# Kernel tuning notes

Hardware: AMD Instinct MI355X
Metric: run time of the kernel (lower is better)

The kernel has to match this reference:

```python
import jax, jax.numpy as jnp
import numpy as np

D = 1024  # input_dim


def setup_inputs() -> dict:
    key = jax.random.key(0)
    ks = jax.random.split(key, 7)
    s = 1.0 / np.sqrt(D)
    return {
        "x": jax.random.normal(ks[0], (4, 2048, D), dtype=jnp.float32),
        "wq": jax.random.normal(ks[1], (D, D), dtype=jnp.float32) * s,
        "bq": jax.random.normal(ks[2], (D,), dtype=jnp.float32) * s,
        "wk": jax.random.normal(ks[3], (D, D), dtype=jnp.float32) * s,
        "bk": jax.random.normal(ks[4], (D,), dtype=jnp.float32) * s,
        "wv": jax.random.normal(ks[5], (D, D), dtype=jnp.float32) * s,
        "bv": jax.random.normal(ks[6], (D,), dtype=jnp.float32) * s,
    }


def reference(x, wq, bq, wk, bk, wv, bv):
    # torch Linear: y = x @ W^T + b
    q = jnp.einsum('btd,ed->bte', x, wq) + bq  # (B,T,D)
    k = jnp.einsum('btd,ed->bte', x, wk) + bk
    v = jnp.einsum('btd,ed->bte', x, wv) + bv
    scale = 1.0 / jnp.sqrt(jnp.asarray(D, dtype=x.dtype))
    scores = jnp.einsum('btd,bsd->bts', q, k) * scale  # (B,T,T)
    attn = jax.nn.softmax(scores, axis=-1)
    return jnp.einsum('bts,bsd->btd', attn, v)
```

## Files before the change

### kernel.cpp

```cpp
#include <hip/hip_runtime.h>
#include <stdint.h>

#define BB 4
#define TT 2048
#define DD 1024

typedef unsigned short u16;
typedef unsigned int u32;
typedef u16 u16x4 __attribute__((ext_vector_type(4)));
typedef u16 u16x8 __attribute__((ext_vector_type(8)));
typedef float f32x4 __attribute__((ext_vector_type(4)));
typedef short s16x8 __attribute__((ext_vector_type(8)));

__device__ __forceinline__ u16 f2bf(float f) {
  u32 u = __float_as_uint(f);
  return (u16)((u + 0x7fffu + ((u >> 16) & 1u)) >> 16);
}
__device__ __forceinline__ float bf2f(u16 h) {
  return __uint_as_float((u32)h << 16);
}

__device__ __forceinline__ void gload_lds16(const void* g, void* l) {
  __builtin_amdgcn_global_load_lds(
      (const __attribute__((address_space(1))) u32*)g,
      (__attribute__((address_space(3))) u32*)l, 16, 0, 0);
}

__device__ __forceinline__ void swizzle_tiles(int& tileM, int& tileN) {
  const int gN = gridDim.x, gM = gridDim.y;
  const int L = blockIdx.y * gN + blockIdx.x;
  const int xcd = L & 7, j = L >> 3;
  const int Mq = gM >> 2, Nq = gN >> 1;
  tileM = (((xcd >> 1) * Mq) + j / Nq) << 7;
  tileN = (((xcd & 1) * Nq) + j % Nq) << 7;
}

__global__ __launch_bounds__(256) void cast_bf16_kernel(
    const float* __restrict__ in, u16* __restrict__ out, int n8) {
  int i = blockIdx.x * 256 + threadIdx.x;
  if (i >= n8) return;
  const f32x4* p = (const f32x4*)in;
  f32x4 a = p[2 * (size_t)i];
  f32x4 b = p[2 * (size_t)i + 1];
  u16x8 o;
  o[0] = f2bf(a[0]); o[1] = f2bf(a[1]); o[2] = f2bf(a[2]); o[3] = f2bf(a[3]);
  o[4] = f2bf(b[0]); o[5] = f2bf(b[1]); o[6] = f2bf(b[2]); o[7] = f2bf(b[3]);
  *(u16x8*)(out + 8 * (size_t)i) = o;
}

__global__ __launch_bounds__(256) void wcast_kernel(
    const float* __restrict__ wq, const float* __restrict__ wk,
    const float* __restrict__ wv, u16* __restrict__ out) {
  int i = blockIdx.x * 256 + threadIdx.x;
  const int n1 = DD * DD / 8;
  const float* src = i < n1 ? wq : (i < 2 * n1 ? wk : wv);
  int ii = i < n1 ? i : (i < 2 * n1 ? i - n1 : i - 2 * n1);
  const f32x4* p = (const f32x4*)src;
  f32x4 a = p[2 * (size_t)ii];
  f32x4 b = p[2 * (size_t)ii + 1];
  u16x8 o;
  o[0] = f2bf(a[0]); o[1] = f2bf(a[1]); o[2] = f2bf(a[2]); o[3] = f2bf(a[3]);
  o[4] = f2bf(b[0]); o[5] = f2bf(b[1]); o[6] = f2bf(b[2]); o[7] = f2bf(b[3]);
  *(u16x8*)(out + 8 * (size_t)i) = o;
}

__global__ __launch_bounds__(256) void bias_concat_kernel(
    const float* __restrict__ bq, const float* __restrict__ bk,
    const float* __restrict__ bv, float* __restrict__ out) {
  int i = blockIdx.x * 256 + threadIdx.x;
  float v = i < DD ? bq[i] : (i < 2 * DD ? bk[i - DD] : bv[i - 2 * DD]);
  out[i] = v;
}

__device__ __forceinline__ void kloop_bt(
    const u16* __restrict__ A, const u16* __restrict__ B, int lda, int ldb,
    int K, int tileM, int tileN, u16* sA, u16* sB, f32x4 acc[4][4]) {
  const int tid = threadIdx.x;
  const int lane = tid & 63;
  const int wave = tid >> 6;
  const int quad = lane >> 4;
  const int l15 = lane & 15;
  const int wm = (wave >> 1) << 6;
  const int wn = (wave & 1) << 6;

  const u16 *gA[4], *gB[4];
  u16 *lA[4], *lB[4];
#pragma unroll
  for (int j = 0; j < 4; ++j) {
    const int ch = wave * 256 + j * 64 + lane;
    const int r = ch >> 3;
    const int cg = ((ch & 7) ^ (r & 7)) * 8;
    gA[j] = A + (size_t)(tileM + r) * lda + cg;
    gB[j] = B + (size_t)(tileN + r) * ldb + cg;
    lA[j] = sA + wave * 2048 + j * 512;
    lB[j] = sB + wave * 2048 + j * 512;
  }

  const int x0 = (quad ^ (l15 & 7)) * 8;
  int aOff[4], bOff[4];
#pragma unroll
  for (int i = 0; i < 4; ++i) {
    aOff[i] = (wm + i * 16 + l15) * 64 + x0;
    bOff[i] = (wn + i * 16 + l15) * 64 + x0;
  }

  for (int it = 0; it < K; it += 64) {
#pragma unroll
    for (int j = 0; j < 4; ++j) gload_lds16(gA[j], lA[j]);
#pragma unroll
    for (int j = 0; j < 4; ++j) gload_lds16(gB[j], lB[j]);
#pragma unroll
    for (int j = 0; j < 4; ++j) { gA[j] += 64; gB[j] += 64; }
    __syncthreads();

    s16x8 af[4], bf[4];
#pragma unroll
    for (int i = 0; i < 4; ++i) af[i] = *(const s16x8*)(sA + aOff[i]);
#pragma unroll
    for (int i = 0; i < 4; ++i) bf[i] = *(const s16x8*)(sB + bOff[i]);
#pragma unroll
    for (int mi = 0; mi < 4; ++mi)
#pragma unroll
      for (int ni = 0; ni < 4; ++ni)
        acc[mi][ni] = __builtin_amdgcn_mfma_f32_16x16x32_bf16(
            af[mi], bf[ni], acc[mi][ni], 0, 0, 0);

#pragma unroll
    for (int i = 0; i < 4; ++i) af[i] = *(const s16x8*)(sA + (aOff[i] ^ 32));
#pragma unroll
    for (int i = 0; i < 4; ++i) bf[i] = *(const s16x8*)(sB + (bOff[i] ^ 32));
#pragma unroll
    for (int mi = 0; mi < 4; ++mi)
#pragma unroll
      for (int ni = 0; ni < 4; ++ni)
        acc[mi][ni] = __builtin_amdgcn_mfma_f32_16x16x32_bf16(
            af[mi], bf[ni], acc[mi][ni], 0, 0, 0);
    __syncthreads();
  }
}

__global__ __launch_bounds__(256, 2) void gemm_qkv(
    const u16* __restrict__ A, const u16* __restrict__ B,
    u16* __restrict__ qk, u16* __restrict__ vt, const float* __restrict__ bias) {
  __shared__ u16 sA[128 * 64];
  __shared__ u16 sB[128 * 64];
  const int lane = threadIdx.x & 63;
  const int wave = threadIdx.x >> 6;
  const int quad = lane >> 4;
  const int l15 = lane & 15;
  const int wm = (wave >> 1) << 6;
  const int wn = (wave & 1) << 6;
  int tileM, tileN;
  swizzle_tiles(tileM, tileN);

  f32x4 acc[4][4] = {};
  kloop_bt(A, B, DD, DD, DD, tileM, tileN, sA, sB, acc);

  const int rowB = tileM + wm + quad * 4;
  const int colB = tileN + wn + l15;
  if (tileN < 2048) {
    const float scale = (tileN < 1024) ? 0.03125f : 1.0f;
#pragma unroll
    for (int mi = 0; mi < 4; ++mi)
#pragma unroll
      for (int r = 0; r < 4; ++r) {
        u16* crow = qk + (size_t)(rowB + mi * 16 + r) * 2048 + colB;
#pragma unroll
        for (int ni = 0; ni < 4; ++ni)
          crow[ni * 16] = f2bf((acc[mi][ni][r] + bias[colB + ni * 16]) * scale);
      }
  } else {
    const int b = tileM >> 11;
    const int tBase = (rowB & 2047);
    u16* vb = vt + (size_t)b * DD * TT;
#pragma unroll
    for (int mi = 0; mi < 4; ++mi)
#pragma unroll
      for (int ni = 0; ni < 4; ++ni) {
        const int e = colB + ni * 16 - 2048;
        const float bs = bias[colB + ni * 16];
        u16x4 o;
#pragma unroll
        for (int r = 0; r < 4; ++r) o[r] = f2bf(acc[mi][ni][r] + bs);
        *(u16x4*)(vb + (size_t)e * TT + tBase + mi * 16) = o;
      }
  }
}

__global__ __launch_bounds__(256, 2) void gemm_s(
    const u16* __restrict__ qk, u16* __restrict__ sbuf,
    float* __restrict__ part) {
  __shared__ u16 sA[128 * 64];
  __shared__ u16 sB[128 * 64];
  const int lane = threadIdx.x & 63;
  const int wave = threadIdx.x >> 6;
  const int quad = lane >> 4;
  const int l15 = lane & 15;
  const int wm = (wave >> 1) << 6;
  const int wn = (wave & 1) << 6;
  int tileM, tileN;
  swizzle_tiles(tileM, tileN);
  const int z = blockIdx.z;

  const u16* A = qk + (size_t)z * TT * 2048;
  const u16* B = qk + (size_t)z * TT * 2048 + 1024;

  f32x4 acc[4][4] = {};
  kloop_bt(A, B, 2048, 2048, 1024, tileM, tileN, sA, sB, acc);

  const int rowB = tileM + wm + quad * 4;
  const int colB = tileN + wn + l15;
  u16* C = sbuf + (size_t)z * TT * 2048;
  const int nIdx2 = (tileN + wn) >> 6;
  float* prow = part + ((size_t)z * 32 + nIdx2) * TT;
#pragma unroll
  for (int mi = 0; mi < 4; ++mi)
#pragma unroll
    for (int r = 0; r < 4; ++r) {
      const int row = rowB + mi * 16 + r;
      u16* crow = C + (size_t)row * 2048 + colB;
      float s = 0.f;
#pragma unroll
      for (int ni = 0; ni < 4; ++ni) {
        const u16 h = f2bf(__expf(acc[mi][ni][r]));
        crow[ni * 16] = h;
        s += bf2f(h);
      }
#pragma unroll
      for (int m = 1; m <= 8; m <<= 1) s += __shfl_xor(s, m, 64);
      if (l15 == 0) prow[row] = s;
    }
}

__global__ __launch_bounds__(256, 2) void gemm_pv(
    const u16* __restrict__ sbuf, const u16* __restrict__ vt,
    float* __restrict__ out, const float* __restrict__ part) {
  __shared__ u16 sA[128 * 64];
  __shared__ u16 sB[128 * 64];
  __shared__ float rowInv[128];
  const int tid = threadIdx.x;
  const int lane = tid & 63;
  const int wave = tid >> 6;
  const int quad = lane >> 4;
  const int l15 = lane & 15;
  const int wm = (wave >> 1) << 6;
  const int wn = (wave & 1) << 6;
  int tileM, tileN;
  swizzle_tiles(tileM, tileN);
  const int z = blockIdx.z;

  if (tid < 128) {
    const float* pp = part + (size_t)z * 32 * TT + tileM + tid;
    float s = 0.f;
#pragma unroll
    for (int j = 0; j < 32; ++j) s += pp[j * TT];
    rowInv[tid] = 1.0f / s;
  }

  const u16* A = sbuf + (size_t)z * TT * 2048;
  const u16* B = vt + (size_t)z * DD * TT;

  f32x4 acc[4][4] = {};
  kloop_bt(A, B, 2048, TT, TT, tileM, tileN, sA, sB, acc);

  const int rowB = tileM + wm + quad * 4;
  const int colB = tileN + wn + l15;
  float* C = out + (size_t)z * TT * DD;
#pragma unroll
  for (int mi = 0; mi < 4; ++mi)
#pragma unroll
    for (int r = 0; r < 4; ++r) {
      const int lrow = wm + quad * 4 + mi * 16 + r;
      const float inv = rowInv[lrow];
      float* crow = C + (size_t)(rowB + mi * 16 + r) * DD + colB;
#pragma unroll
      for (int ni = 0; ni < 4; ++ni) crow[ni * 16] = acc[mi][ni][r] * inv;
    }
}

extern "C" void kernel_launch(void* const* d_in, const int* in_sizes, int n_in,
                              void* d_out, int out_size, void* d_ws,
                              size_t ws_size, hipStream_t stream) {
  const float* x = (const float*)d_in[0];
  const float* wq = (const float*)d_in[1];
  const float* bq = (const float*)d_in[2];
  const float* wk = (const float*)d_in[3];
  const float* bk = (const float*)d_in[4];
  const float* wv = (const float*)d_in[5];
  const float* bv = (const float*)d_in[6];
  float* out = (float*)d_out;

  const size_t MB = 1024 * 1024;
  if (ws_size < 103 * MB) return;
  char* ws = (char*)d_ws;
  u16* xbf = (u16*)(ws);
  float* part = (float*)(ws);
  u16* wcat = (u16*)(ws + 16 * MB);
  float* bcat = (float*)(ws + 22 * MB);
  u16* qk = (u16*)(ws + 23 * MB);
  u16* vt = (u16*)(ws + 55 * MB);
  u16* sbuf = (u16*)(ws + 71 * MB);

  const dim3 blk(256);

  cast_bf16_kernel<<<BB * TT * DD / 8 / 256, blk, 0, stream>>>(
      x, xbf, BB * TT * DD / 8);
  wcast_kernel<<<3 * DD * DD / 8 / 256, blk, 0, stream>>>(wq, wk, wv, wcat);
  bias_concat_kernel<<<12, blk, 0, stream>>>(bq, bk, bv, bcat);

  gemm_qkv<<<dim3(3 * DD / 128, BB * TT / 128, 1), blk, 0, stream>>>(
      xbf, wcat, qk, vt, bcat);

  gemm_s<<<dim3(TT / 128, TT / 128, BB), blk, 0, stream>>>(qk, sbuf, part);

  gemm_pv<<<dim3(DD / 128, TT / 128, BB), blk, 0, stream>>>(
      sbuf, vt, out, part);
}
```

Measured before the change: 236.1 us.

## Use 256x128 tiles with 8 waves and triple-buffered LDS pipeline in GEMMs

All three GEMMs move from 128x128 tiles with 4 waves to 256x128 tiles with 8 waves (512 threads). The k-loop becomes a 3-stage LDS ring buffer that prefetches two tiles ahead. Global-to-LDS loads are interleaved between MFMA quarter-blocks, with explicit waitcnt, barriers and setprio. The goal is to hide global-load latency and raise reuse of the B operand. The cost is 144 KB of LDS per block (likely one block per CU) and many more barriers, which may limit occupancy.

```diff
diff --git a/kernel.cpp b/kernel.cpp
--- a/kernel.cpp
+++ b/kernel.cpp
@@ -31,7 +31,7 @@
   const int L = blockIdx.y * gN + blockIdx.x;
   const int xcd = L & 7, j = L >> 3;
   const int Mq = gM >> 2, Nq = gN >> 1;
-  tileM = (((xcd >> 1) * Mq) + j / Nq) << 7;
+  tileM = (((xcd >> 1) * Mq) + j / Nq) << 8;
   tileN = (((xcd & 1) * Nq) + j % Nq) << 7;
 }
 
@@ -72,9 +72,33 @@
   out[i] = v;
 }
 
-__device__ __forceinline__ void kloop_bt(
+#define BUFE 24576
+
+__device__ __forceinline__ void ld2(const u16* sb, const int* off,
+                                    s16x8 out[2][2]) {
+#pragma unroll
+  for (int i = 0; i < 2; ++i) {
+    out[i][0] = *(const s16x8*)(sb + off[i]);
+    out[i][1] = *(const s16x8*)(sb + (off[i] ^ 32));
+  }
+}
+
+__device__ __forceinline__ void mfma8(const s16x8 af[2][2],
+                                      const s16x8 bf[2][2], f32x4 acc[4][4],
+                                      int mo, int no) {
+#pragma unroll
+  for (int mi = 0; mi < 2; ++mi)
+#pragma unroll
+    for (int ni = 0; ni < 2; ++ni)
+#pragma unroll
+      for (int ks = 0; ks < 2; ++ks)
+        acc[mo + mi][no + ni] = __builtin_amdgcn_mfma_f32_16x16x32_bf16(
+            af[mi][ks], bf[ni][ks], acc[mo + mi][no + ni], 0, 0, 0);
+}
+
+__device__ __forceinline__ void kloop8(
     const u16* __restrict__ A, const u16* __restrict__ B, int lda, int ldb,
-    int K, int tileM, int tileN, u16* sA, u16* sB, f32x4 acc[4][4]) {
+    int K, int tileM, int tileN, u16* sm, f32x4 acc[4][4]) {
   const int tid = threadIdx.x;
   const int lane = tid & 63;
   const int wave = tid >> 6;
@@ -83,17 +107,24 @@
   const int wm = (wave >> 1) << 6;
   const int wn = (wave & 1) << 6;
 
-  const u16 *gA[4], *gB[4];
-  u16 *lA[4], *lB[4];
+  const u16* gA[4];
+  const u16* gB[2];
+  int lA[4], lB[2];
 #pragma unroll
   for (int j = 0; j < 4; ++j) {
     const int ch = wave * 256 + j * 64 + lane;
     const int r = ch >> 3;
     const int cg = ((ch & 7) ^ (r & 7)) * 8;
     gA[j] = A + (size_t)(tileM + r) * lda + cg;
+    lA[j] = wave * 2048 + j * 512;
+  }
+#pragma unroll
+  for (int j = 0; j < 2; ++j) {
+    const int ch = wave * 128 + j * 64 + lane;
+    const int r = ch >> 3;
+    const int cg = ((ch & 7) ^ (r & 7)) * 8;
     gB[j] = B + (size_t)(tileN + r) * ldb + cg;
-    lA[j] = sA + wave * 2048 + j * 512;
-    lB[j] = sB + wave * 2048 + j * 512;
+    lB[j] = 16384 + wave * 1024 + j * 512;
   }
 
   const int x0 = (quad ^ (l15 & 7)) * 8;
@@ -101,49 +132,86 @@
 #pragma unroll
   for (int i = 0; i < 4; ++i) {
     aOff[i] = (wm + i * 16 + l15) * 64 + x0;
-    bOff[i] = (wn + i * 16 + l15) * 64 + x0;
-  }
-
-  for (int it = 0; it < K; it += 64) {
-#pragma unroll
-    for (int j = 0; j < 4; ++j) gload_lds16(gA[j], lA[j]);
-#pragma unroll
-    for (int j = 0; j < 4; ++j) gload_lds16(gB[j], lB[j]);
-#pragma unroll
-    for (int j = 0; j < 4; ++j) { gA[j] += 64; gB[j] += 64; }
-    __syncthreads();
-
-    s16x8 af[4], bf[4];
-#pragma unroll
-    for (int i = 0; i < 4; ++i) af[i] = *(const s16x8*)(sA + aOff[i]);
-#pragma unroll
-    for (int i = 0; i < 4; ++i) bf[i] = *(const s16x8*)(sB + bOff[i]);
-#pragma unroll
-    for (int mi = 0; mi < 4; ++mi)
-#pragma unroll
-      for (int ni = 0; ni < 4; ++ni)
-        acc[mi][ni] = __builtin_amdgcn_mfma_f32_16x16x32_bf16(
-            af[mi], bf[ni], acc[mi][ni], 0, 0, 0);
-
-#pragma unroll
-    for (int i = 0; i < 4; ++i) af[i] = *(const s16x8*)(sA + (aOff[i] ^ 32));
-#pragma unroll
-    for (int i = 0; i < 4; ++i) bf[i] = *(const s16x8*)(sB + (bOff[i] ^ 32));
-#pragma unroll
-    for (int mi = 0; mi < 4; ++mi)
-#pragma unroll
-      for (int ni = 0; ni < 4; ++ni)
-        acc[mi][ni] = __builtin_amdgcn_mfma_f32_16x16x32_bf16(
-            af[mi], bf[ni], acc[mi][ni], 0, 0, 0);
-    __syncthreads();
-  }
-}
-
-__global__ __launch_bounds__(256, 2) void gemm_qkv(
+    bOff[i] = 16384 + (wn + i * 16 + l15) * 64 + x0;
+  }
+
+#pragma unroll
+  for (int tb = 0; tb < 2; ++tb) {
+    u16* dst = sm + tb * BUFE;
+#pragma unroll
+    for (int j = 0; j < 4; ++j) gload_lds16(gA[j], dst + lA[j]);
+#pragma unroll
+    for (int j = 0; j < 2; ++j) gload_lds16(gB[j], dst + lB[j]);
+#pragma unroll
+    for (int j = 0; j < 4; ++j) gA[j] += 64;
+#pragma unroll
+    for (int j = 0; j < 2; ++j) gB[j] += 64;
+  }
+  asm volatile("s_waitcnt vmcnt(6)");
+  __builtin_amdgcn_s_barrier();
+
+  const int NT = K >> 6;
+  int buf = 0;
+  for (int t = 0; t < NT; ++t) {
+    const u16* sb = sm + buf * BUFE;
+    const int b2i = (buf + 2 >= 3) ? buf - 1 : buf + 2;
+    u16* st = sm + b2i * BUFE;
+    const bool stage = (t + 2 < NT);
+
+    s16x8 fa0[2][2], fb0[2][2], fa2[2][2], fb2[2][2];
+
+    ld2(sb, aOff, fa0);
+    ld2(sb, bOff, fb0);
+    if (stage) { gload_lds16(gA[0], st + lA[0]); gload_lds16(gA[1], st + lA[1]); }
+    __builtin_amdgcn_s_barrier();
+    asm volatile("s_waitcnt lgkmcnt(0)");
+    __builtin_amdgcn_s_setprio(1);
+    mfma8(fa0, fb0, acc, 0, 0);
+    __builtin_amdgcn_s_setprio(0);
+    __builtin_amdgcn_s_barrier();
+
+    ld2(sb, bOff + 2, fb2);
+    if (stage) { gload_lds16(gA[2], st + lA[2]); gload_lds16(gA[3], st + lA[3]); }
+    __builtin_amdgcn_s_barrier();
+    asm volatile("s_waitcnt lgkmcnt(0)");
+    __builtin_amdgcn_s_setprio(1);
+    mfma8(fa0, fb2, acc, 0, 2);
+    __builtin_amdgcn_s_setprio(0);
+    __builtin_amdgcn_s_barrier();
+
+    ld2(sb, aOff + 2, fa2);
+    if (stage) {
+      gload_lds16(gB[0], st + lB[0]);
+      gload_lds16(gB[1], st + lB[1]);
+#pragma unroll
+      for (int j = 0; j < 4; ++j) gA[j] += 64;
+#pragma unroll
+      for (int j = 0; j < 2; ++j) gB[j] += 64;
+    }
+    __builtin_amdgcn_s_barrier();
+    asm volatile("s_waitcnt lgkmcnt(0)");
+    __builtin_amdgcn_s_setprio(1);
+    mfma8(fa2, fb2, acc, 2, 2);
+    __builtin_amdgcn_s_setprio(0);
+    __builtin_amdgcn_s_barrier();
+
+    __builtin_amdgcn_s_setprio(1);
+    mfma8(fa2, fb0, acc, 2, 0);
+    __builtin_amdgcn_s_setprio(0);
+    if (t < NT - 2) {
+      asm volatile("s_waitcnt vmcnt(6)");
+    } else if (t == NT - 2) {
+      asm volatile("s_waitcnt vmcnt(0)");
+    }
+    __builtin_amdgcn_s_barrier();
+    buf = (buf + 1 >= 3) ? 0 : buf + 1;
+  }
+}
+
+__global__ __launch_bounds__(512, 2) void gemm_qkv(
     const u16* __restrict__ A, const u16* __restrict__ B,
     u16* __restrict__ qk, u16* __restrict__ vt, const float* __restrict__ bias) {
-  __shared__ u16 sA[128 * 64];
-  __shared__ u16 sB[128 * 64];
+  __shared__ u16 sm[3 * BUFE];
   const int lane = threadIdx.x & 63;
   const int wave = threadIdx.x >> 6;
   const int quad = lane >> 4;
@@ -154,7 +222,7 @@
   swizzle_tiles(tileM, tileN);
 
   f32x4 acc[4][4] = {};
-  kloop_bt(A, B, DD, DD, DD, tileM, tileN, sA, sB, acc);
+  kloop8(A, B, DD, DD, DD, tileM, tileN, sm, acc);
 
   const int rowB = tileM + wm + quad * 4;
   const int colB = tileN + wn + l15;
@@ -187,11 +255,10 @@
   }
 }
 
-__global__ __launch_bounds__(256, 2) void gemm_s(
+__global__ __launch_bounds__(512, 2) void gemm_s(
     const u16* __restrict__ qk, u16* __restrict__ sbuf,
     float* __restrict__ part) {
-  __shared__ u16 sA[128 * 64];
-  __shared__ u16 sB[128 * 64];
+  __shared__ u16 sm[3 * BUFE];
   const int lane = threadIdx.x & 63;
   const int wave = threadIdx.x >> 6;
   const int quad = lane >> 4;
@@ -206,7 +273,7 @@
   const u16* B = qk + (size_t)z * TT * 2048 + 1024;
 
   f32x4 acc[4][4] = {};
-  kloop_bt(A, B, 2048, 2048, 1024, tileM, tileN, sA, sB, acc);
+  kloop8(A, B, 2048, 2048, 1024, tileM, tileN, sm, acc);
 
   const int rowB = tileM + wm + quad * 4;
   const int colB = tileN + wn + l15;
@@ -232,12 +299,11 @@
     }
 }
 
-__global__ __launch_bounds__(256, 2) void gemm_pv(
+__global__ __launch_bounds__(512, 2) void gemm_pv(
     const u16* __restrict__ sbuf, const u16* __restrict__ vt,
     float* __restrict__ out, const float* __restrict__ part) {
-  __shared__ u16 sA[128 * 64];
-  __shared__ u16 sB[128 * 64];
-  __shared__ float rowInv[128];
+  __shared__ u16 sm[3 * BUFE];
+  __shared__ float rowInv[256];
   const int tid = threadIdx.x;
   const int lane = tid & 63;
   const int wave = tid >> 6;
@@ -249,19 +315,20 @@
   swizzle_tiles(tileM, tileN);
   const int z = blockIdx.z;
 
-  if (tid < 128) {
+  if (tid < 256) {
     const float* pp = part + (size_t)z * 32 * TT + tileM + tid;
     float s = 0.f;
 #pragma unroll
     for (int j = 0; j < 32; ++j) s += pp[j * TT];
     rowInv[tid] = 1.0f / s;
   }
+  __syncthreads();
 
   const u16* A = sbuf + (size_t)z * TT * 2048;
   const u16* B = vt + (size_t)z * DD * TT;
 
   f32x4 acc[4][4] = {};
-  kloop_bt(A, B, 2048, TT, TT, tileM, tileN, sA, sB, acc);
+  kloop8(A, B, 2048, TT, TT, tileM, tileN, sm, acc);
 
   const int rowB = tileM + wm + quad * 4;
   const int colB = tileN + wn + l15;
@@ -301,18 +368,19 @@
   u16* vt = (u16*)(ws + 55 * MB);
   u16* sbuf = (u16*)(ws + 71 * MB);
 
-  const dim3 blk(256);
-
-  cast_bf16_kernel<<<BB * TT * DD / 8 / 256, blk, 0, stream>>>(
+  const dim3 blk256(256);
+  const dim3 blk512(512);
+
+  cast_bf16_kernel<<<BB * TT * DD / 8 / 256, blk256, 0, stream>>>(
       x, xbf, BB * TT * DD / 8);
-  wcast_kernel<<<3 * DD * DD / 8 / 256, blk, 0, stream>>>(wq, wk, wv, wcat);
-  bias_concat_kernel<<<12, blk, 0, stream>>>(bq, bk, bv, bcat);
-
-  gemm_qkv<<<dim3(3 * DD / 128, BB * TT / 128, 1), blk, 0, stream>>>(
+  wcast_kernel<<<3 * DD * DD / 8 / 256, blk256, 0, stream>>>(wq, wk, wv, wcat);
+  bias_concat_kernel<<<12, blk256, 0, stream>>>(bq, bk, bv, bcat);
+
+  gemm_qkv<<<dim3(3 * DD / 128, BB * TT / 256, 1), blk512, 0, stream>>>(
       xbf, wcat, qk, vt, bcat);
 
-  gemm_s<<<dim3(TT / 128, TT / 128, BB), blk, 0, stream>>>(qk, sbuf, part);
-
-  gemm_pv<<<dim3(DD / 128, TT / 128, BB), blk, 0, stream>>>(
+  gemm_s<<<dim3(TT / 128, TT / 256, BB), blk512, 0, stream>>>(qk, sbuf, part);
+
+  gemm_pv<<<dim3(DD / 128, TT / 256, BB), blk512, 0, stream>>>(
       sbuf, vt, out, part);
 }
```

Measured after the change: 259.4 us. +9.9%, slower.

## Use 256-row, 8-wave GEMM tiles with interleaved load/MFMA pipeline for QKV and scores

Applied to the files above, without the earlier changes.

Adds a new 512-thread k-loop that computes 256x192 (QKV) or 256x256 (scores) tiles with double-buffered LDS. Global-to-LDS loads are split into four phases interleaved with MFMA bursts, using explicit barriers, waitcnts and setprio. The goal is more operand reuse per byte loaded and better overlap of memory with compute. It costs more LDS and registers per block, fewer blocks in the grid, and a fragile hand-written sync schedule. The PV GEMM keeps the old 128x128 path.

```diff
diff --git a/kernel.cpp b/kernel.cpp
--- a/kernel.cpp
+++ b/kernel.cpp
@@ -26,13 +26,13 @@
       (__attribute__((address_space(3))) u32*)l, 16, 0, 0);
 }
 
-__device__ __forceinline__ void swizzle_tiles(int& tileM, int& tileN) {
+__device__ __forceinline__ void swz(int BMv, int BNv, int& tileM, int& tileN) {
   const int gN = gridDim.x, gM = gridDim.y;
   const int L = blockIdx.y * gN + blockIdx.x;
   const int xcd = L & 7, j = L >> 3;
   const int Mq = gM >> 2, Nq = gN >> 1;
-  tileM = (((xcd >> 1) * Mq) + j / Nq) << 7;
-  tileN = (((xcd & 1) * Nq) + j % Nq) << 7;
+  tileM = (((xcd >> 1) * Mq) + j / Nq) * BMv;
+  tileN = (((xcd & 1) * Nq) + j % Nq) * BNv;
 }
 
 __global__ __launch_bounds__(256) void cast_bf16_kernel(
@@ -72,6 +72,163 @@
   out[i] = v;
 }
 
+template <int NR>
+__device__ __forceinline__ void kloop256(
+    const u16* __restrict__ A, const u16* __restrict__ B, int lda, int ldb,
+    int K, int tileM, int tileN, u16* sm, f32x4 (&acc)[8][NR]) {
+  constexpr int AE = 16384;
+  constexpr int BUF = AE + NR * 4096;
+  const int tid = threadIdx.x;
+  const int lane = tid & 63;
+  const int wave = tid >> 6;
+  const int quad = lane >> 4;
+  const int l15 = lane & 15;
+  const int wm = (wave >> 2) << 7;
+  const int wn = (wave & 3) * (NR * 16);
+
+  const int chl = wave * 64 + lane;
+  const int rloc = chl >> 3;
+  const int cg = ((chl & 7) ^ (rloc & 7)) * 8;
+  const int ldst = chl * 8;
+
+  const u16* gA[4];
+  const u16* gB[NR];
+#pragma unroll
+  for (int j = 0; j < 4; ++j)
+    gA[j] = A + (size_t)(tileM + j * 64 + rloc) * lda + cg;
+#pragma unroll
+  for (int j = 0; j < NR; ++j)
+    gB[j] = B + (size_t)(tileN + j * 64 + rloc) * ldb + cg;
+
+  const int x0 = (quad ^ (l15 & 7)) * 8;
+  int aOff[8];
+  int bOff[NR];
+#pragma unroll
+  for (int i = 0; i < 8; ++i) aOff[i] = (wm + i * 16 + l15) * 64 + x0;
+#pragma unroll
+  for (int i = 0; i < NR; ++i) bOff[i] = AE + (wn + i * 16 + l15) * 64 + x0;
+
+  {
+    u16* d = sm;
+    gload_lds16(gA[0], d + 0 * 4096 + ldst);
+    gload_lds16(gA[2], d + 2 * 4096 + ldst);
+#pragma unroll
+    for (int j = 0; j < NR; ++j) gload_lds16(gB[j], d + AE + j * 4096 + ldst);
+    gload_lds16(gA[1], d + 1 * 4096 + ldst);
+    gload_lds16(gA[3], d + 3 * 4096 + ldst);
+#pragma unroll
+    for (int j = 0; j < 4; ++j) gA[j] += 64;
+#pragma unroll
+    for (int j = 0; j < NR; ++j) gB[j] += 64;
+  }
+  asm volatile("s_waitcnt vmcnt(2)" ::: "memory");
+  __builtin_amdgcn_s_barrier();
+  __builtin_amdgcn_sched_barrier(0);
+
+  const int NT = K >> 6;
+  for (int t = 0; t < NT; ++t) {
+    const u16* sb = sm + (t & 1) * BUF;
+    u16* st = sm + ((t + 1) & 1) * BUF;
+    const bool stg = (t + 1 < NT);
+    s16x8 af[4], bf[NR];
+
+#pragma unroll
+    for (int i = 0; i < 4; ++i) af[i] = *(const s16x8*)(sb + aOff[i]);
+#pragma unroll
+    for (int i = 0; i < NR; ++i) bf[i] = *(const s16x8*)(sb + bOff[i]);
+    if (stg) {
+      gload_lds16(gA[0], st + 0 * 4096 + ldst);
+      gload_lds16(gA[2], st + 2 * 4096 + ldst);
+    }
+    __builtin_amdgcn_s_barrier();
+    __builtin_amdgcn_sched_barrier(0);
+    asm volatile("s_waitcnt lgkmcnt(0)" ::: "memory");
+    __builtin_amdgcn_s_setprio(1);
+#pragma unroll
+    for (int mi = 0; mi < 4; ++mi)
+#pragma unroll
+      for (int ni = 0; ni < NR; ++ni)
+        acc[mi][ni] = __builtin_amdgcn_mfma_f32_16x16x32_bf16(
+            af[mi], bf[ni], acc[mi][ni], 0, 0, 0);
+    __builtin_amdgcn_s_setprio(0);
+    if (stg) {
+      asm volatile("s_waitcnt vmcnt(2)" ::: "memory");
+    } else {
+      asm volatile("s_waitcnt vmcnt(0)" ::: "memory");
+    }
+    __builtin_amdgcn_s_barrier();
+    __builtin_amdgcn_sched_barrier(0);
+
+#pragma unroll
+    for (int i = 0; i < 4; ++i) af[i] = *(const s16x8*)(sb + aOff[4 + i]);
+    if (stg) {
+      gload_lds16(gB[0], st + AE + 0 * 4096 + ldst);
+      gload_lds16(gB[1], st + AE + 1 * 4096 + ldst);
+    }
+    __builtin_amdgcn_s_barrier();
+    __builtin_amdgcn_sched_barrier(0);
+    asm volatile("s_waitcnt lgkmcnt(0)" ::: "memory");
+    __builtin_amdgcn_s_setprio(1);
+#pragma unroll
+    for (int mi = 0; mi < 4; ++mi)
+#pragma unroll
+      for (int ni = 0; ni < NR; ++ni)
+        acc[4 + mi][ni] = __builtin_amdgcn_mfma_f32_16x16x32_bf16(
+            af[mi], bf[ni], acc[4 + mi][ni], 0, 0, 0);
+    __builtin_amdgcn_s_setprio(0);
+    __builtin_amdgcn_s_barrier();
+    __builtin_amdgcn_sched_barrier(0);
+
+#pragma unroll
+    for (int i = 0; i < 4; ++i) af[i] = *(const s16x8*)(sb + (aOff[i] ^ 32));
+#pragma unroll
+    for (int i = 0; i < NR; ++i) bf[i] = *(const s16x8*)(sb + (bOff[i] ^ 32));
+    if (stg) {
+      gload_lds16(gB[2], st + AE + 2 * 4096 + ldst);
+      if constexpr (NR == 4) gload_lds16(gB[3], st + AE + 3 * 4096 + ldst);
+    }
+    __builtin_amdgcn_s_barrier();
+    __builtin_amdgcn_sched_barrier(0);
+    asm volatile("s_waitcnt lgkmcnt(0)" ::: "memory");
+    __builtin_amdgcn_s_setprio(1);
+#pragma unroll
+    for (int mi = 0; mi < 4; ++mi)
+#pragma unroll
+      for (int ni = 0; ni < NR; ++ni)
+        acc[mi][ni] = __builtin_amdgcn_mfma_f32_16x16x32_bf16(
+            af[mi], bf[ni], acc[mi][ni], 0, 0, 0);
+    __builtin_amdgcn_s_setprio(0);
+    __builtin_amdgcn_s_barrier();
+    __builtin_amdgcn_sched_barrier(0);
+
+#pragma unroll
+    for (int i = 0; i < 4; ++i)
+      af[i] = *(const s16x8*)(sb + (aOff[4 + i] ^ 32));
+    if (stg) {
+      gload_lds16(gA[1], st + 1 * 4096 + ldst);
+      gload_lds16(gA[3], st + 3 * 4096 + ldst);
+#pragma unroll
+      for (int j = 0; j < 4; ++j) gA[j] += 64;
+#pragma unroll
+      for (int j = 0; j < NR; ++j) gB[j] += 64;
+    }
+    __builtin_amdgcn_s_barrier();
+    __builtin_amdgcn_sched_barrier(0);
+    asm volatile("s_waitcnt lgkmcnt(0)" ::: "memory");
+    __builtin_amdgcn_s_setprio(1);
+#pragma unroll
+    for (int mi = 0; mi < 4; ++mi)
+#pragma unroll
+      for (int ni = 0; ni < NR; ++ni)
+        acc[4 + mi][ni] = __builtin_amdgcn_mfma_f32_16x16x32_bf16(
+            af[mi], bf[ni], acc[4 + mi][ni], 0, 0, 0);
+    __builtin_amdgcn_s_setprio(0);
+    if (stg) asm volatile("s_waitcnt vmcnt(2)" ::: "memory");
+    __builtin_amdgcn_s_barrier();
+    __builtin_amdgcn_sched_barrier(0);
+  }
+}
+
 __device__ __forceinline__ void kloop_bt(
     const u16* __restrict__ A, const u16* __restrict__ B, int lda, int ldb,
     int K, int tileM, int tileN, u16* sA, u16* sB, f32x4 acc[4][4]) {
@@ -139,74 +296,70 @@
   }
 }
 
-__global__ __launch_bounds__(256, 2) void gemm_qkv(
+__global__ __launch_bounds__(512, 2) void gemm_qkv(
     const u16* __restrict__ A, const u16* __restrict__ B,
     u16* __restrict__ qk, u16* __restrict__ vt, const float* __restrict__ bias) {
-  __shared__ u16 sA[128 * 64];
-  __shared__ u16 sB[128 * 64];
+  __shared__ u16 sm[2 * (16384 + 3 * 4096)];
   const int lane = threadIdx.x & 63;
   const int wave = threadIdx.x >> 6;
   const int quad = lane >> 4;
   const int l15 = lane & 15;
-  const int wm = (wave >> 1) << 6;
-  const int wn = (wave & 1) << 6;
+  const int wm = (wave >> 2) << 7;
+  const int wn = (wave & 3) * 48;
   int tileM, tileN;
-  swizzle_tiles(tileM, tileN);
-
-  f32x4 acc[4][4] = {};
-  kloop_bt(A, B, DD, DD, DD, tileM, tileN, sA, sB, acc);
+  swz(256, 192, tileM, tileN);
+
+  f32x4 acc[8][3] = {};
+  kloop256<3>(A, B, DD, DD, DD, tileM, tileN, sm, acc);
 
   const int rowB = tileM + wm + quad * 4;
-  const int colB = tileN + wn + l15;
-  if (tileN < 2048) {
-    const float scale = (tileN < 1024) ? 0.03125f : 1.0f;
-#pragma unroll
-    for (int mi = 0; mi < 4; ++mi)
-#pragma unroll
-      for (int r = 0; r < 4; ++r) {
-        u16* crow = qk + (size_t)(rowB + mi * 16 + r) * 2048 + colB;
-#pragma unroll
-        for (int ni = 0; ni < 4; ++ni)
-          crow[ni * 16] = f2bf((acc[mi][ni][r] + bias[colB + ni * 16]) * scale);
+#pragma unroll
+  for (int ni = 0; ni < 3; ++ni) {
+    const int c0 = tileN + wn + ni * 16;
+    const int col = c0 + l15;
+    const float bs = bias[col];
+    if (c0 < 2048) {
+      const float scale = c0 < 1024 ? 0.03125f : 1.0f;
+#pragma unroll
+      for (int mi = 0; mi < 8; ++mi)
+#pragma unroll
+        for (int r = 0; r < 4; ++r)
+          qk[(size_t)(rowB + mi * 16 + r) * 2048 + col] =
+              f2bf((acc[mi][ni][r] + bs) * scale);
+    } else {
+      const int b = tileM >> 11;
+      const int tBase = rowB & 2047;
+      u16* vb = vt + (size_t)b * DD * TT + (size_t)(col - 2048) * TT;
+#pragma unroll
+      for (int mi = 0; mi < 8; ++mi) {
+        u16x4 o;
+#pragma unroll
+        for (int r = 0; r < 4; ++r) o[r] = f2bf(acc[mi][ni][r] + bs);
+        *(u16x4*)(vb + tBase + mi * 16) = o;
       }
-  } else {
-    const int b = tileM >> 11;
-    const int tBase = (rowB & 2047);
-    u16* vb = vt + (size_t)b * DD * TT;
-#pragma unroll
-    for (int mi = 0; mi < 4; ++mi)
-#pragma unroll
-      for (int ni = 0; ni < 4; ++ni) {
-        const int e = colB + ni * 16 - 2048;
-        const float bs = bias[colB + ni * 16];
-        u16x4 o;
-#pragma unroll
-        for (int r = 0; r < 4; ++r) o[r] = f2bf(acc[mi][ni][r] + bs);
-        *(u16x4*)(vb + (size_t)e * TT + tBase + mi * 16) = o;
-      }
-  }
-}
-
-__global__ __launch_bounds__(256, 2) void gemm_s(
+    }
+  }
+}
+
+__global__ __launch_bounds__(512, 2) void gemm_s(
     const u16* __restrict__ qk, u16* __restrict__ sbuf,
     float* __restrict__ part) {
-  __shared__ u16 sA[128 * 64];
-  __shared__ u16 sB[128 * 64];
+  __shared__ u16 sm[2 * (16384 + 4 * 4096)];
   const int lane = threadIdx.x & 63;
   const int wave = threadIdx.x >> 6;
   const int quad = lane >> 4;
   const int l15 = lane & 15;
-  const int wm = (wave >> 1) << 6;
-  const int wn = (wave & 1) << 6;
+  const int wm = (wave >> 2) << 7;
+  const int wn = (wave & 3) << 6;
   int tileM, tileN;
-  swizzle_tiles(tileM, tileN);
+  swz(256, 256, tileM, tileN);
   const int z = blockIdx.z;
 
   const u16* A = qk + (size_t)z * TT * 2048;
   const u16* B = qk + (size_t)z * TT * 2048 + 1024;
 
-  f32x4 acc[4][4] = {};
-  kloop_bt(A, B, 2048, 2048, 1024, tileM, tileN, sA, sB, acc);
+  f32x4 acc[8][4] = {};
+  kloop256<4>(A, B, 2048, 2048, 1024, tileM, tileN, sm, acc);
 
   const int rowB = tileM + wm + quad * 4;
   const int colB = tileN + wn + l15;
@@ -214,7 +367,7 @@
   const int nIdx2 = (tileN + wn) >> 6;
   float* prow = part + ((size_t)z * 32 + nIdx2) * TT;
 #pragma unroll
-  for (int mi = 0; mi < 4; ++mi)
+  for (int mi = 0; mi < 8; ++mi)
 #pragma unroll
     for (int r = 0; r < 4; ++r) {
       const int row = rowB + mi * 16 + r;
@@ -246,7 +399,7 @@
   const int wm = (wave >> 1) << 6;
   const int wn = (wave & 1) << 6;
   int tileM, tileN;
-  swizzle_tiles(tileM, tileN);
+  swz(128, 128, tileM, tileN);
   const int z = blockIdx.z;
 
   if (tid < 128) {
@@ -301,18 +454,19 @@
   u16* vt = (u16*)(ws + 55 * MB);
   u16* sbuf = (u16*)(ws + 71 * MB);
 
-  const dim3 blk(256);
-
-  cast_bf16_kernel<<<BB * TT * DD / 8 / 256, blk, 0, stream>>>(
+  const dim3 blk256(256);
+  const dim3 blk512(512);
+
+  cast_bf16_kernel<<<BB * TT * DD / 8 / 256, blk256, 0, stream>>>(
       x, xbf, BB * TT * DD / 8);
-  wcast_kernel<<<3 * DD * DD / 8 / 256, blk, 0, stream>>>(wq, wk, wv, wcat);
-  bias_concat_kernel<<<12, blk, 0, stream>>>(bq, bk, bv, bcat);
-
-  gemm_qkv<<<dim3(3 * DD / 128, BB * TT / 128, 1), blk, 0, stream>>>(
+  wcast_kernel<<<3 * DD * DD / 8 / 256, blk256, 0, stream>>>(wq, wk, wv, wcat);
+  bias_concat_kernel<<<12, blk256, 0, stream>>>(bq, bk, bv, bcat);
+
+  gemm_qkv<<<dim3(3 * DD / 192, BB * TT / 256, 1), blk512, 0, stream>>>(
       xbf, wcat, qk, vt, bcat);
 
-  gemm_s<<<dim3(TT / 128, TT / 128, BB), blk, 0, stream>>>(qk, sbuf, part);
-
-  gemm_pv<<<dim3(DD / 128, TT / 128, BB), blk, 0, stream>>>(
+  gemm_s<<<dim3(TT / 256, TT / 256, BB), blk512, 0, stream>>>(qk, sbuf, part);
+
+  gemm_pv<<<dim3(DD / 128, TT / 128, BB), blk256, 0, stream>>>(
       sbuf, vt, out, part);
 }
```

Result: no change. 240.5 us (+1.9%).

## Double-buffer LDS k-loop for score and PV GEMMs and fuse prep kernels

Applied to the files above, without the earlier changes.

Adds a double-buffered k-loop in which async global-to-LDS loads for tile t+2 are issued while MFMAs run on the current tile. It uses vmcnt-based waits, explicit barriers and raised wave priority around the MFMA block. gemm_s and gemm_pv switch to this loop with 64KB of shared memory. The three cast and concat kernels are merged into one launch. The larger LDS footprint may limit occupancy to 2 blocks per CU, and the hand-written waitcnt logic is fragile.

```diff
diff --git a/kernel.cpp b/kernel.cpp
--- a/kernel.cpp
+++ b/kernel.cpp
@@ -26,50 +26,50 @@
       (__attribute__((address_space(3))) u32*)l, 16, 0, 0);
 }
 
-__device__ __forceinline__ void swizzle_tiles(int& tileM, int& tileN) {
+__device__ __forceinline__ void swz(int BMv, int BNv, int& tileM, int& tileN) {
   const int gN = gridDim.x, gM = gridDim.y;
   const int L = blockIdx.y * gN + blockIdx.x;
   const int xcd = L & 7, j = L >> 3;
   const int Mq = gM >> 2, Nq = gN >> 1;
-  tileM = (((xcd >> 1) * Mq) + j / Nq) << 7;
-  tileN = (((xcd & 1) * Nq) + j % Nq) << 7;
-}
-
-__global__ __launch_bounds__(256) void cast_bf16_kernel(
-    const float* __restrict__ in, u16* __restrict__ out, int n8) {
+  tileM = (((xcd >> 1) * Mq) + j / Nq) * BMv;
+  tileN = (((xcd & 1) * Nq) + j % Nq) * BNv;
+}
+
+__global__ __launch_bounds__(256) void prep_kernel(
+    const float* __restrict__ x, const float* __restrict__ wq,
+    const float* __restrict__ wk, const float* __restrict__ wv,
+    const float* __restrict__ bq, const float* __restrict__ bk,
+    const float* __restrict__ bv, u16* __restrict__ xbf,
+    u16* __restrict__ wcat, float* __restrict__ bcat) {
+  const int NX = BB * TT * DD / 8;
+  const int NW = DD * DD / 8;
   int i = blockIdx.x * 256 + threadIdx.x;
-  if (i >= n8) return;
-  const f32x4* p = (const f32x4*)in;
-  f32x4 a = p[2 * (size_t)i];
-  f32x4 b = p[2 * (size_t)i + 1];
-  u16x8 o;
-  o[0] = f2bf(a[0]); o[1] = f2bf(a[1]); o[2] = f2bf(a[2]); o[3] = f2bf(a[3]);
-  o[4] = f2bf(b[0]); o[5] = f2bf(b[1]); o[6] = f2bf(b[2]); o[7] = f2bf(b[3]);
-  *(u16x8*)(out + 8 * (size_t)i) = o;
-}
-
-__global__ __launch_bounds__(256) void wcast_kernel(
-    const float* __restrict__ wq, const float* __restrict__ wk,
-    const float* __restrict__ wv, u16* __restrict__ out) {
-  int i = blockIdx.x * 256 + threadIdx.x;
-  const int n1 = DD * DD / 8;
-  const float* src = i < n1 ? wq : (i < 2 * n1 ? wk : wv);
-  int ii = i < n1 ? i : (i < 2 * n1 ? i - n1 : i - 2 * n1);
-  const f32x4* p = (const f32x4*)src;
-  f32x4 a = p[2 * (size_t)ii];
-  f32x4 b = p[2 * (size_t)ii + 1];
-  u16x8 o;
-  o[0] = f2bf(a[0]); o[1] = f2bf(a[1]); o[2] = f2bf(a[2]); o[3] = f2bf(a[3]);
-  o[4] = f2bf(b[0]); o[5] = f2bf(b[1]); o[6] = f2bf(b[2]); o[7] = f2bf(b[3]);
-  *(u16x8*)(out + 8 * (size_t)i) = o;
-}
-
-__global__ __launch_bounds__(256) void bias_concat_kernel(
-    const float* __restrict__ bq, const float* __restrict__ bk,
-    const float* __restrict__ bv, float* __restrict__ out) {
-  int i = blockIdx.x * 256 + threadIdx.x;
-  float v = i < DD ? bq[i] : (i < 2 * DD ? bk[i - DD] : bv[i - 2 * DD]);
-  out[i] = v;
+  if (i < NX) {
+    const f32x4* p = (const f32x4*)x;
+    f32x4 a = p[2 * (size_t)i];
+    f32x4 b = p[2 * (size_t)i + 1];
+    u16x8 o;
+    o[0] = f2bf(a[0]); o[1] = f2bf(a[1]); o[2] = f2bf(a[2]); o[3] = f2bf(a[3]);
+    o[4] = f2bf(b[0]); o[5] = f2bf(b[1]); o[6] = f2bf(b[2]); o[7] = f2bf(b[3]);
+    *(u16x8*)(xbf + 8 * (size_t)i) = o;
+  } else if (i < NX + 3 * NW) {
+    const int k = i - NX;
+    const float* src = k < NW ? wq : (k < 2 * NW ? wk : wv);
+    const int ii = k < NW ? k : (k < 2 * NW ? k - NW : k - 2 * NW);
+    const f32x4* p = (const f32x4*)src;
+    f32x4 a = p[2 * (size_t)ii];
+    f32x4 b = p[2 * (size_t)ii + 1];
+    u16x8 o;
+    o[0] = f2bf(a[0]); o[1] = f2bf(a[1]); o[2] = f2bf(a[2]); o[3] = f2bf(a[3]);
+    o[4] = f2bf(b[0]); o[5] = f2bf(b[1]); o[6] = f2bf(b[2]); o[7] = f2bf(b[3]);
+    *(u16x8*)(wcat + 8 * (size_t)k) = o;
+  } else {
+    const int k = i - NX - 3 * NW;
+    if (k < 3 * DD) {
+      float v = k < DD ? bq[k] : (k < 2 * DD ? bk[k - DD] : bv[k - 2 * DD]);
+      bcat[k] = v;
+    }
+  }
 }
 
 __device__ __forceinline__ void kloop_bt(
@@ -136,6 +136,102 @@
         acc[mi][ni] = __builtin_amdgcn_mfma_f32_16x16x32_bf16(
             af[mi], bf[ni], acc[mi][ni], 0, 0, 0);
     __syncthreads();
+  }
+}
+
+__device__ __forceinline__ void kloop_dbc(
+    const u16* __restrict__ A, const u16* __restrict__ B, int lda, int ldb,
+    int K, int tileM, int tileN, u16* sm, f32x4 acc[4][4]) {
+  const int tid = threadIdx.x;
+  const int lane = tid & 63;
+  const int wave = tid >> 6;
+  const int quad = lane >> 4;
+  const int l15 = lane & 15;
+  const int wm = (wave >> 1) << 6;
+  const int wn = (wave & 1) << 6;
+
+  const u16 *gA[4], *gB[4];
+  int lA[4], lB[4];
+#pragma unroll
+  for (int j = 0; j < 4; ++j) {
+    const int ch = wave * 256 + j * 64 + lane;
+    const int r = ch >> 3;
+    const int cg = ((ch & 7) ^ (r & 7)) * 8;
+    gA[j] = A + (size_t)(tileM + r) * lda + cg;
+    gB[j] = B + (size_t)(tileN + r) * ldb + cg;
+    lA[j] = wave * 2048 + j * 512;
+    lB[j] = 8192 + wave * 2048 + j * 512;
+  }
+
+  const int x0 = (quad ^ (l15 & 7)) * 8;
+  int aOff[4], bOff[4];
+#pragma unroll
+  for (int i = 0; i < 4; ++i) {
+    aOff[i] = (wm + i * 16 + l15) * 64 + x0;
+    bOff[i] = 8192 + (wn + i * 16 + l15) * 64 + x0;
+  }
+
+#pragma unroll
+  for (int p = 0; p < 2; ++p) {
+    u16* d = sm + p * 16384;
+#pragma unroll
+    for (int j = 0; j < 4; ++j) gload_lds16(gA[j], d + lA[j]);
+#pragma unroll
+    for (int j = 0; j < 4; ++j) gload_lds16(gB[j], d + lB[j]);
+#pragma unroll
+    for (int j = 0; j < 4; ++j) { gA[j] += 64; gB[j] += 64; }
+  }
+
+  const int NT = K >> 6;
+  for (int t = 0; t < NT; ++t) {
+    const u16* sb = sm + (t & 1) * 16384;
+    u16* st = sm + (t & 1) * 16384;
+
+    if (t + 1 < NT) {
+      asm volatile("s_waitcnt vmcnt(8)" ::: "memory");
+    } else {
+      asm volatile("s_waitcnt vmcnt(0)" ::: "memory");
+    }
+    __builtin_amdgcn_s_barrier();
+    __builtin_amdgcn_sched_barrier(0);
+
+    s16x8 a0[4], b0[4], a1[4], b1[4];
+#pragma unroll
+    for (int i = 0; i < 4; ++i) a0[i] = *(const s16x8*)(sb + aOff[i]);
+#pragma unroll
+    for (int i = 0; i < 4; ++i) b0[i] = *(const s16x8*)(sb + bOff[i]);
+#pragma unroll
+    for (int i = 0; i < 4; ++i) a1[i] = *(const s16x8*)(sb + (aOff[i] ^ 32));
+#pragma unroll
+    for (int i = 0; i < 4; ++i) b1[i] = *(const s16x8*)(sb + (bOff[i] ^ 32));
+    asm volatile("s_waitcnt lgkmcnt(0)" ::: "memory");
+    __builtin_amdgcn_sched_barrier(0);
+    __builtin_amdgcn_s_barrier();
+    __builtin_amdgcn_sched_barrier(0);
+
+    if (t + 2 < NT) {
+#pragma unroll
+      for (int j = 0; j < 4; ++j) gload_lds16(gA[j], st + lA[j]);
+#pragma unroll
+      for (int j = 0; j < 4; ++j) gload_lds16(gB[j], st + lB[j]);
+#pragma unroll
+      for (int j = 0; j < 4; ++j) { gA[j] += 64; gB[j] += 64; }
+    }
+
+    __builtin_amdgcn_s_setprio(1);
+#pragma unroll
+    for (int mi = 0; mi < 4; ++mi)
+#pragma unroll
+      for (int ni = 0; ni < 4; ++ni)
+        acc[mi][ni] = __builtin_amdgcn_mfma_f32_16x16x32_bf16(
+            a0[mi], b0[ni], acc[mi][ni], 0, 0, 0);
+#pragma unroll
+    for (int mi = 0; mi < 4; ++mi)
+#pragma unroll
+      for (int ni = 0; ni < 4; ++ni)
+        acc[mi][ni] = __builtin_amdgcn_mfma_f32_16x16x32_bf16(
+            a1[mi], b1[ni], acc[mi][ni], 0, 0, 0);
+    __builtin_amdgcn_s_setprio(0);
   }
 }
 
@@ -151,7 +247,7 @@
   const int wm = (wave >> 1) << 6;
   const int wn = (wave & 1) << 6;
   int tileM, tileN;
-  swizzle_tiles(tileM, tileN);
+  swz(128, 128, tileM, tileN);
 
   f32x4 acc[4][4] = {};
   kloop_bt(A, B, DD, DD, DD, tileM, tileN, sA, sB, acc);
@@ -190,8 +286,7 @@
 __global__ __launch_bounds__(256, 2) void gemm_s(
     const u16* __restrict__ qk, u16* __restrict__ sbuf,
     float* __restrict__ part) {
-  __shared__ u16 sA[128 * 64];
-  __shared__ u16 sB[128 * 64];
+  __shared__ u16 sm[2 * 16384];
   const int lane = threadIdx.x & 63;
   const int wave = threadIdx.x >> 6;
   const int quad = lane >> 4;
@@ -199,14 +294,14 @@
   const int wm = (wave >> 1) << 6;
   const int wn = (wave & 1) << 6;
   int tileM, tileN;
-  swizzle_tiles(tileM, tileN);
+  swz(128, 128, tileM, tileN);
   const int z = blockIdx.z;
 
   const u16* A = qk + (size_t)z * TT * 2048;
   const u16* B = qk + (size_t)z * TT * 2048 + 1024;
 
   f32x4 acc[4][4] = {};
-  kloop_bt(A, B, 2048, 2048, 1024, tileM, tileN, sA, sB, acc);
+  kloop_dbc(A, B, 2048, 2048, 1024, tileM, tileN, sm, acc);
 
   const int rowB = tileM + wm + quad * 4;
   const int colB = tileN + wn + l15;
@@ -235,8 +330,7 @@
 __global__ __launch_bounds__(256, 2) void gemm_pv(
     const u16* __restrict__ sbuf, const u16* __restrict__ vt,
     float* __restrict__ out, const float* __restrict__ part) {
-  __shared__ u16 sA[128 * 64];
-  __shared__ u16 sB[128 * 64];
+  __shared__ u16 sm[2 * 16384];
   __shared__ float rowInv[128];
   const int tid = threadIdx.x;
   const int lane = tid & 63;
@@ -246,7 +340,7 @@
   const int wm = (wave >> 1) << 6;
   const int wn = (wave & 1) << 6;
   int tileM, tileN;
-  swizzle_tiles(tileM, tileN);
+  swz(128, 128, tileM, tileN);
   const int z = blockIdx.z;
 
   if (tid < 128) {
@@ -256,12 +350,13 @@
     for (int j = 0; j < 32; ++j) s += pp[j * TT];
     rowInv[tid] = 1.0f / s;
   }
+  __syncthreads();
 
   const u16* A = sbuf + (size_t)z * TT * 2048;
   const u16* B = vt + (size_t)z * DD * TT;
 
   f32x4 acc[4][4] = {};
-  kloop_bt(A, B, 2048, TT, TT, tileM, tileN, sA, sB, acc);
+  kloop_dbc(A, B, 2048, TT, TT, tileM, tileN, sm, acc);
 
   const int rowB = tileM + wm + quad * 4;
   const int colB = tileN + wn + l15;
@@ -301,18 +396,16 @@
   u16* vt = (u16*)(ws + 55 * MB);
   u16* sbuf = (u16*)(ws + 71 * MB);
 
-  const dim3 blk(256);
-
-  cast_bf16_kernel<<<BB * TT * DD / 8 / 256, blk, 0, stream>>>(
-      x, xbf, BB * TT * DD / 8);
-  wcast_kernel<<<3 * DD * DD / 8 / 256, blk, 0, stream>>>(wq, wk, wv, wcat);
-  bias_concat_kernel<<<12, blk, 0, stream>>>(bq, bk, bv, bcat);
-
-  gemm_qkv<<<dim3(3 * DD / 128, BB * TT / 128, 1), blk, 0, stream>>>(
+  const dim3 blk256(256);
+
+  prep_kernel<<<4096 + 1536 + 12, blk256, 0, stream>>>(
+      x, wq, wk, wv, bq, bk, bv, xbf, wcat, bcat);
+
+  gemm_qkv<<<dim3(3 * DD / 128, BB * TT / 128, 1), blk256, 0, stream>>>(
       xbf, wcat, qk, vt, bcat);
 
-  gemm_s<<<dim3(TT / 128, TT / 128, BB), blk, 0, stream>>>(qk, sbuf, part);
-
-  gemm_pv<<<dim3(DD / 128, TT / 128, BB), blk, 0, stream>>>(
+  gemm_s<<<dim3(TT / 128, TT / 128, BB), blk256, 0, stream>>>(qk, sbuf, part);
+
+  gemm_pv<<<dim3(DD / 128, TT / 128, BB), blk256, 0, stream>>>(
       sbuf, vt, out, part);
 }
```

Result: faster. 231.1 us, median of 3 (-2.1%).
